# Optimization experiments

Measured on AMD Instinct MI355X. Metric: run time of the kernel, lower is better.

## Reference

```python
import jax, jax.numpy as jnp
import numpy as np

VOCAB, EMB, HID, B, T = 32000, 256, 256, 64, 2048


def setup_inputs() -> dict:
    key = jax.random.key(0)
    ks = jax.random.split(key, 6)
    s = 1.0 / np.sqrt(HID)
    return {
        "source": jax.random.randint(ks[0], (B, T), 0, VOCAB),
        "embedding": jax.random.normal(ks[1], (VOCAB, EMB), dtype=jnp.float32) * 0.02,
        "W_ih": jax.random.uniform(ks[2], (EMB, HID), jnp.float32, -s, s),
        "W_hh": jax.random.uniform(ks[3], (HID, HID), jnp.float32, -s, s),
        "b_ih": jax.random.uniform(ks[4], (HID,), jnp.float32, -s, s),
        "b_hh": jax.random.uniform(ks[5], (HID,), jnp.float32, -s, s),
    }


def reference(source, embedding, W_ih, W_hh, b_ih, b_hh):
    # embedding lookup: [B, T, EMB]
    embedded = embedding[source]
    # scan over time with carried hidden state (RNNCellManual: tanh cell)
    xs = jnp.swapaxes(embedded, 0, 1)  # [T, B, EMB]

    def step(h, x_t):
        h_new = jnp.tanh(x_t @ W_ih + b_ih + h @ W_hh + b_hh)
        return h_new, None

    h0 = jnp.zeros((source.shape[0], W_hh.shape[0]), dtype=embedding.dtype)
    h_T, _ = jax.lax.scan(step, h0, xs)
    return h_T  # final hidden state [B, HID]
```

## Files before the change

kernel.cpp:

```cpp
#include <hip/hip_runtime.h>

#define TT 2048
#define BB 64
#define HH 256

typedef _Float16 half2_t __attribute__((ext_vector_type(2)));
typedef _Float16 half8_t __attribute__((ext_vector_type(8)));
typedef float f32x4 __attribute__((ext_vector_type(4)));
typedef int i32x4 __attribute__((ext_vector_type(4)));

__global__ void prep_kernel(const float* __restrict__ Wih, const float* __restrict__ Whh,
                            _Float16* __restrict__ WihT, _Float16* __restrict__ WhhT) {
  const int n = blockIdx.x;
  const int k = threadIdx.x;
  WihT[n * HH + k] = (_Float16)Wih[k * HH + n];
  WhhT[n * HH + k] = (_Float16)Whh[k * HH + n];
}

__global__ __launch_bounds__(256, 2) void embed_gemm_kernel(
    const int* __restrict__ source, const float* __restrict__ emb,
    const _Float16* __restrict__ WihT, const float* __restrict__ b_ih,
    const float* __restrict__ b_hh, _Float16* __restrict__ U) {
  const int t = blockIdx.x;
  const int nbase = blockIdx.y * 64;
  __shared__ __align__(16) _Float16 Bs[64][280];

  const int tid = threadIdx.x;
  for (int c = tid; c < 64 * 32; c += 256) {
    const int n = c >> 5;
    const int ko = (c & 31) * 8;
    *(half8_t*)&Bs[n][ko] = *(const half8_t*)(WihT + (size_t)(nbase + n) * HH + ko);
  }
  __syncthreads();

  const int lane = tid & 63;
  const int wave = tid >> 6;
  const int row16 = lane & 15;
  const int quad = lane >> 4;
  const int b = wave * 16 + row16;
  const int src = source[b * TT + t];
  const float* arow = emb + (size_t)src * HH + quad * 8;

  f32x4 acc[4];
#pragma unroll
  for (int ct = 0; ct < 4; ++ct) acc[ct] = (f32x4){0.f, 0.f, 0.f, 0.f};

#pragma unroll
  for (int kt = 0; kt < 8; ++kt) {
    const float4 x0 = *(const float4*)(arow + kt * 32);
    const float4 x1 = *(const float4*)(arow + kt * 32 + 4);
    half8_t af;
    af[0] = (_Float16)x0.x; af[1] = (_Float16)x0.y;
    af[2] = (_Float16)x0.z; af[3] = (_Float16)x0.w;
    af[4] = (_Float16)x1.x; af[5] = (_Float16)x1.y;
    af[6] = (_Float16)x1.z; af[7] = (_Float16)x1.w;
#pragma unroll
    for (int ct = 0; ct < 4; ++ct) {
      const half8_t bf = *(const half8_t*)&Bs[ct * 16 + row16][quad * 8 + kt * 32];
      acc[ct] = __builtin_amdgcn_mfma_f32_16x16x32_f16(af, bf, acc[ct], 0, 0, 0);
    }
  }

#pragma unroll
  for (int ct = 0; ct < 4; ++ct) {
    const int nn = nbase + ct * 16 + row16;
    const float bias = b_ih[nn] + b_hh[nn];
#pragma unroll
    for (int r = 0; r < 4; ++r) {
      const int bb = wave * 16 + quad * 4 + r;
      U[((size_t)t * BB + bb) * HH + nn] = (_Float16)(acc[ct][r] + bias);
    }
  }
}

__global__ __launch_bounds__(256)
__attribute__((amdgpu_waves_per_eu(1, 1)))
void rnn_scan_kernel(
    const _Float16* __restrict__ U, const _Float16* __restrict__ WhhT,
    float* __restrict__ out) {
  const int b = blockIdx.x;
  const int tid = threadIdx.x;
  const int w = tid >> 6;
  const int l = tid & 63;
  const int col = l & 15;
  const int quad = l >> 4;

  __shared__ __align__(16) _Float16 hbuf[2][HH];

  half8_t wb[4][8];
#pragma unroll
  for (int tt = 0; tt < 4; ++tt) {
    const _Float16* base = WhhT + (size_t)(64 * w + 16 * tt + col) * HH + quad * 8;
#pragma unroll
    for (int c = 0; c < 8; ++c) wb[tt][c] = *(const half8_t*)(base + 32 * c);
  }
  asm volatile("" : "+a"(wb[0][0]), "+a"(wb[0][1]), "+a"(wb[0][2]), "+a"(wb[0][3]),
                    "+a"(wb[0][4]), "+a"(wb[0][5]), "+a"(wb[0][6]), "+a"(wb[0][7]),
                    "+a"(wb[1][0]), "+a"(wb[1][1]), "+a"(wb[1][2]), "+a"(wb[1][3]),
                    "+a"(wb[1][4]), "+a"(wb[1][5]), "+a"(wb[1][6]), "+a"(wb[1][7]));
  asm volatile("" : "+a"(wb[2][0]), "+a"(wb[2][1]), "+a"(wb[2][2]), "+a"(wb[2][3]),
                    "+a"(wb[2][4]), "+a"(wb[2][5]), "+a"(wb[2][6]), "+a"(wb[2][7]),
                    "+a"(wb[3][0]), "+a"(wb[3][1]), "+a"(wb[3][2]), "+a"(wb[3][3]),
                    "+a"(wb[3][4]), "+a"(wb[3][5]), "+a"(wb[3][6]), "+a"(wb[3][7]));

  hbuf[0][tid] = (_Float16)0.f;

  const _Float16* Up = U + b * HH + tid;
  _Float16 uc[8], un[8];
#pragma unroll
  for (int s = 0; s < 8; ++s) uc[s] = Up[(size_t)s * (BB * HH)];

  float hn = 0.f;
  __syncthreads();

  for (int tc = 0; tc < TT; tc += 8) {
    const int tn = (tc + 8) & (TT - 1);
#pragma unroll
    for (int s = 0; s < 8; ++s) un[s] = Up[(size_t)(tn + s) * (BB * HH)];

#pragma unroll
    for (int s = 0; s < 8; ++s) {
      const int t = tc + s;

      const _Float16* hrow = hbuf[t & 1] + quad * 8;
      half8_t ha[8];
#pragma unroll
      for (int c = 0; c < 8; ++c) ha[c] = *(const half8_t*)(hrow + 32 * c);
      asm volatile("" : "+v"(ha[0]), "+v"(ha[1]), "+v"(ha[2]), "+v"(ha[3]),
                        "+v"(ha[4]), "+v"(ha[5]), "+v"(ha[6]), "+v"(ha[7]));

      f32x4 cacc[4];
#pragma unroll
      for (int tt = 0; tt < 4; ++tt) cacc[tt] = (f32x4){0.f, 0.f, 0.f, 0.f};
#pragma unroll
      for (int c = 0; c < 8; ++c)
#pragma unroll
        for (int tt = 0; tt < 4; ++tt)
          cacc[tt] = __builtin_amdgcn_mfma_f32_16x16x32_f16(ha[c], wb[tt][c], cacc[tt], 0, 0, 0);

      float y = cacc[0][0];
      y = (quad == 1) ? cacc[1][0] : y;
      y = (quad == 2) ? cacc[2][0] : y;
      y = (quad == 3) ? cacc[3][0] : y;

      const float a = (float)uc[s] + y;
      const float e = __builtin_amdgcn_exp2f(a * 2.885390081777927f);
      hn = 1.f - 2.f * __builtin_amdgcn_rcpf(e + 1.f);
      hbuf[(t + 1) & 1][tid] = (_Float16)hn;

      __syncthreads();
    }
#pragma unroll
    for (int s = 0; s < 8; ++s) uc[s] = un[s];
  }
  out[(size_t)b * HH + tid] = hn;
}

extern "C" void kernel_launch(void* const* d_in, const int* in_sizes, int n_in,
                              void* d_out, int out_size, void* d_ws, size_t ws_size,
                              hipStream_t stream) {
  const int*   source = (const int*)d_in[0];
  const float* emb    = (const float*)d_in[1];
  const float* Wih    = (const float*)d_in[2];
  const float* Whh    = (const float*)d_in[3];
  const float* bih    = (const float*)d_in[4];
  const float* bhh    = (const float*)d_in[5];
  float* out = (float*)d_out;

  char* ws = (char*)d_ws;
  _Float16* U    = (_Float16*)ws;
  _Float16* WihT = (_Float16*)(ws + 67108864);
  _Float16* WhhT = (_Float16*)(ws + 67239936);

  prep_kernel<<<dim3(256), dim3(256), 0, stream>>>(Wih, Whh, WihT, WhhT);
  embed_gemm_kernel<<<dim3(TT, 4), dim3(256), 0, stream>>>(source, emb, WihT, bih, bhh, U);
  rnn_scan_kernel<<<dim3(BB), dim3(256), 0, stream>>>(U, WhhT, out);
}
```

Measured before the change: 946.2 us.

## Split recurrent matvec between MFMA and packed-dot paths in scan kernel

The recurrent W_hh product in the scan kernel is divided so that 192 output columns go through MFMA (3 tiles per wave instead of 4) and 64 columns are computed with v_dot2 fp16 dot products plus DPP lane reductions. The aim is to shorten the per-timestep MFMA dependency chain by running VALU work in parallel with the matrix unit. The U staging also moves from per-thread registers into a double-buffered LDS buffer, so each thread can read whichever column it owns. The cost is more register pressure and LDS traffic, plus a more complex indexing scheme.

```diff
diff --git a/kernel.cpp b/kernel.cpp
--- a/kernel.cpp
+++ b/kernel.cpp
@@ -8,6 +8,11 @@
 typedef _Float16 half8_t __attribute__((ext_vector_type(8)));
 typedef float f32x4 __attribute__((ext_vector_type(4)));
 typedef int i32x4 __attribute__((ext_vector_type(4)));
+
+static __device__ __forceinline__ float dot2i(int h, int w, float acc) {
+  return __builtin_amdgcn_fdot2(__builtin_bit_cast(half2_t, h),
+                                __builtin_bit_cast(half2_t, w), acc, false);
+}
 
 __global__ void prep_kernel(const float* __restrict__ Wih, const float* __restrict__ Whh,
                             _Float16* __restrict__ WihT, _Float16* __restrict__ WhhT) {
@@ -82,15 +87,16 @@
   const int tid = threadIdx.x;
   const int w = tid >> 6;
   const int l = tid & 63;
-  const int col = l & 15;
-  const int quad = l >> 4;
+  const int col = l & 15, quad = l >> 4;
+  const int jo = l >> 2, kk = l & 3;
 
   __shared__ __align__(16) _Float16 hbuf[2][HH];
-
-  half8_t wb[4][8];
-#pragma unroll
-  for (int tt = 0; tt < 4; ++tt) {
-    const _Float16* base = WhhT + (size_t)(64 * w + 16 * tt + col) * HH + quad * 8;
+  __shared__ __align__(16) _Float16 ubuf[2][8 * HH];
+
+  half8_t wb[3][8];
+#pragma unroll
+  for (int tt = 0; tt < 3; ++tt) {
+    const _Float16* base = WhhT + (size_t)(64 + 48 * w + 16 * tt + col) * HH + quad * 8;
 #pragma unroll
     for (int c = 0; c < 8; ++c) wb[tt][c] = *(const half8_t*)(base + 32 * c);
   }
@@ -99,61 +105,102 @@
                     "+a"(wb[1][0]), "+a"(wb[1][1]), "+a"(wb[1][2]), "+a"(wb[1][3]),
                     "+a"(wb[1][4]), "+a"(wb[1][5]), "+a"(wb[1][6]), "+a"(wb[1][7]));
   asm volatile("" : "+a"(wb[2][0]), "+a"(wb[2][1]), "+a"(wb[2][2]), "+a"(wb[2][3]),
-                    "+a"(wb[2][4]), "+a"(wb[2][5]), "+a"(wb[2][6]), "+a"(wb[2][7]),
-                    "+a"(wb[3][0]), "+a"(wb[3][1]), "+a"(wb[3][2]), "+a"(wb[3][3]),
-                    "+a"(wb[3][4]), "+a"(wb[3][5]), "+a"(wb[3][6]), "+a"(wb[3][7]));
+                    "+a"(wb[2][4]), "+a"(wb[2][5]), "+a"(wb[2][6]), "+a"(wb[2][7]));
+
+  i32x4 wr[8];
+  {
+    const _Float16* base = WhhT + (size_t)(16 * w + jo) * HH + 64 * kk;
+#pragma unroll
+    for (int i = 0; i < 8; ++i) wr[i] = *(const i32x4*)(base + 8 * ((i + 2 * kk) & 7));
+  }
+  asm volatile("" : "+v"(wr[0]), "+v"(wr[1]), "+v"(wr[2]), "+v"(wr[3]),
+                    "+v"(wr[4]), "+v"(wr[5]), "+v"(wr[6]), "+v"(wr[7]));
 
   hbuf[0][tid] = (_Float16)0.f;
 
-  const _Float16* Up = U + b * HH + tid;
-  _Float16 uc[8], un[8];
-#pragma unroll
-  for (int s = 0; s < 8; ++s) uc[s] = Up[(size_t)s * (BB * HH)];
-
-  float hn = 0.f;
+  const int n_m = (64 + 48 * w + 16 * quad + col) & 255;
+  const int n_d = 16 * w + jo;
+
+  {
+#pragma unroll
+    for (int s = 0; s < 8; ++s)
+      ubuf[0][s * HH + tid] = U[((size_t)s * BB + b) * HH + tid];
+  }
+  float hn_m = 0.f, hn_d = 0.f;
   __syncthreads();
 
   for (int tc = 0; tc < TT; tc += 8) {
     const int tn = (tc + 8) & (TT - 1);
-#pragma unroll
-    for (int s = 0; s < 8; ++s) un[s] = Up[(size_t)(tn + s) * (BB * HH)];
+    _Float16 ut[8];
+#pragma unroll
+    for (int s = 0; s < 8; ++s)
+      ut[s] = U[((size_t)(tn + s) * BB + b) * HH + tid];
 
 #pragma unroll
     for (int s = 0; s < 8; ++s) {
       const int t = tc + s;
-
-      const _Float16* hrow = hbuf[t & 1] + quad * 8;
+      const _Float16* hb = hbuf[t & 1];
+
       half8_t ha[8];
 #pragma unroll
-      for (int c = 0; c < 8; ++c) ha[c] = *(const half8_t*)(hrow + 32 * c);
+      for (int c = 0; c < 8; ++c) ha[c] = *(const half8_t*)(hb + 32 * c + quad * 8);
+      i32x4 hv[8];
+#pragma unroll
+      for (int i = 0; i < 8; ++i)
+        hv[i] = *(const i32x4*)(hb + 64 * kk + 8 * ((i + 2 * kk) & 7));
       asm volatile("" : "+v"(ha[0]), "+v"(ha[1]), "+v"(ha[2]), "+v"(ha[3]),
                         "+v"(ha[4]), "+v"(ha[5]), "+v"(ha[6]), "+v"(ha[7]));
-
-      f32x4 cacc[4];
-#pragma unroll
-      for (int tt = 0; tt < 4; ++tt) cacc[tt] = (f32x4){0.f, 0.f, 0.f, 0.f};
+      asm volatile("" : "+v"(hv[0]), "+v"(hv[1]), "+v"(hv[2]), "+v"(hv[3]),
+                        "+v"(hv[4]), "+v"(hv[5]), "+v"(hv[6]), "+v"(hv[7]));
+
+      f32x4 cacc[3];
+#pragma unroll
+      for (int tt = 0; tt < 3; ++tt) cacc[tt] = (f32x4){0.f, 0.f, 0.f, 0.f};
 #pragma unroll
       for (int c = 0; c < 8; ++c)
 #pragma unroll
-        for (int tt = 0; tt < 4; ++tt)
+        for (int tt = 0; tt < 3; ++tt)
           cacc[tt] = __builtin_amdgcn_mfma_f32_16x16x32_f16(ha[c], wb[tt][c], cacc[tt], 0, 0, 0);
 
-      float y = cacc[0][0];
-      y = (quad == 1) ? cacc[1][0] : y;
-      y = (quad == 2) ? cacc[2][0] : y;
-      y = (quad == 3) ? cacc[3][0] : y;
-
-      const float a = (float)uc[s] + y;
-      const float e = __builtin_amdgcn_exp2f(a * 2.885390081777927f);
-      hn = 1.f - 2.f * __builtin_amdgcn_rcpf(e + 1.f);
-      hbuf[(t + 1) & 1][tid] = (_Float16)hn;
-
+      float pa0 = 0.f, pa1 = 0.f, pa2 = 0.f, pa3 = 0.f;
+#pragma unroll
+      for (int i = 0; i < 8; ++i) {
+        const i32x4 h4 = hv[i];
+        const i32x4 w4 = wr[i];
+        pa0 = dot2i(h4[0], w4[0], pa0);
+        pa1 = dot2i(h4[1], w4[1], pa1);
+        pa2 = dot2i(h4[2], w4[2], pa2);
+        pa3 = dot2i(h4[3], w4[3], pa3);
+      }
+      float pa = (pa0 + pa1) + (pa2 + pa3);
+      pa += __int_as_float(__builtin_amdgcn_mov_dpp(__float_as_int(pa), 0xB1, 0xF, 0xF, true));
+      pa += __int_as_float(__builtin_amdgcn_mov_dpp(__float_as_int(pa), 0x4E, 0xF, 0xF, true));
+
+      float ym = cacc[0][0];
+      ym = (quad == 1) ? cacc[1][0] : ym;
+      ym = (quad == 2) ? cacc[2][0] : ym;
+      const float um = (float)ubuf[(tc >> 3) & 1][s * HH + n_m];
+      const float am = um + ym;
+      const float em = __builtin_amdgcn_exp2f(am * 2.885390081777927f);
+      hn_m = 1.f - 2.f * __builtin_amdgcn_rcpf(em + 1.f);
+      if (quad < 3) hbuf[(t + 1) & 1][n_m] = (_Float16)hn_m;
+
+      const float ud = (float)ubuf[(tc >> 3) & 1][s * HH + n_d];
+      const float ad = ud + pa;
+      const float ed = __builtin_amdgcn_exp2f(ad * 2.885390081777927f);
+      hn_d = 1.f - 2.f * __builtin_amdgcn_rcpf(ed + 1.f);
+      if (kk == 0) hbuf[(t + 1) & 1][n_d] = (_Float16)hn_d;
+
+      if (s == 0) {
+#pragma unroll
+        for (int q = 0; q < 8; ++q)
+          ubuf[((tc >> 3) + 1) & 1][q * HH + tid] = ut[q];
+      }
       __syncthreads();
     }
-#pragma unroll
-    for (int s = 0; s < 8; ++s) uc[s] = un[s];
-  }
-  out[(size_t)b * HH + tid] = hn;
+  }
+  if (quad < 3) out[(size_t)b * HH + n_m] = hn_m;
+  if (kk == 0)  out[(size_t)b * HH + n_d] = hn_d;
 }
 
 extern "C" void kernel_launch(void* const* d_in, const int* in_sizes, int n_in,
```

New measurement: 1.411 ms. 1.49x slower.
